# Optimization experiments

Measured on AMD Instinct MI355X. Metric: run time of the kernel, lower is better.

The kernel has to match this reference:

```python
import jax, jax.numpy as jnp
import numpy as np

B, S, D, H = 4, 2048, 1024, 16
Dh = D // H


def _layernorm(x, a, b):
    # torch.var default is unbiased (ddof=1)
    mu = jnp.mean(x, axis=-1, keepdims=True)
    sg = jnp.var(x, axis=-1, keepdims=True, ddof=1)
    return (x - mu) / jnp.sqrt(sg + 1e-08) * a + b


def setup_inputs() -> dict:
    key = jax.random.key(0)
    ks = jax.random.split(key, 16)
    s = 1.0 / np.sqrt(D)
    inp = {
        'q': jax.random.normal(ks[0], (B, S, D), jnp.float32),
        'k': jax.random.normal(ks[1], (B, S, D), jnp.float32),
        'v': jax.random.normal(ks[2], (B, S, D), jnp.float32),
        'g': jax.random.normal(ks[3], (B, S, D), jnp.float32),
        # causal mask: True = masked
        'm': jnp.triu(jnp.ones((S, S), jnp.bool_), k=1)[None, None],
        'Wq': jax.random.uniform(ks[4], (D, D), jnp.float32, -s, s),
        'bq': jnp.zeros((D,), jnp.float32),
        'Wk': jax.random.uniform(ks[5], (D, D), jnp.float32, -s, s),
        'bk': jnp.zeros((D,), jnp.float32),
        'Wv': jax.random.uniform(ks[6], (D, D), jnp.float32, -s, s),
        'bv': jnp.zeros((D,), jnp.float32),
        'Wg': jax.random.uniform(ks[7], (D, D), jnp.float32, -s, s),
        'bg': jnp.zeros((D,), jnp.float32),
        'ln_a': jnp.ones((D,), jnp.float32),
        'ln_b': jnp.zeros((D,), jnp.float32),
        'Wo': jax.random.uniform(ks[8], (D, D), jnp.float32, -s, s),
        'bo': jnp.zeros((D,), jnp.float32),
    }
    return inp


def reference(q, k, v, g, m, Wq, bq, Wk, bk, Wv, bv, Wg, bg, ln_a, ln_b, Wo, bo):
    qp = q @ Wq.T + bq
    kp = k @ Wk.T + bk
    vp = v @ Wv.T + bv
    gp = g @ Wg.T + bg
    # gating path: exact GELU (torch default), then custom LayerNorm (unbiased var)
    vp = jax.nn.gelu(vp, approximate=False)
    gp = jax.nn.gelu(gp, approximate=False)
    vp = _layernorm(vp, ln_a, ln_b)
    # [B,S,D] -> [B,H,S,Dh]
    qh = qp.reshape(B, S, H, Dh).transpose(0, 2, 1, 3)
    kh = kp.reshape(B, S, H, Dh).transpose(0, 2, 1, 3)
    vh = vp.reshape(B, S, H, Dh).transpose(0, 2, 1, 3)
    gh = gp.reshape(B, S, H, Dh).transpose(0, 2, 1, 3)
    a = jnp.einsum('bhqd,bhkd->bhqk', qh, kh) / jnp.sqrt(jnp.float32(Dh))
    a = jnp.where(m, -jnp.inf, a)
    a = jax.nn.softmax(a, axis=-1)
    # dropout = 0.0 (inference): no-op
    o = jnp.einsum('bhqk,bhkd->bhqd', a, vh)
    o = o * gh
    o = o.transpose(0, 2, 1, 3).reshape(B, S, D)
    o = o @ Wo.T + bo
    return (o, a)
```

## Files before the change

### kernel.cpp

```cpp
#include <hip/hip_runtime.h>
#include <hip/hip_bf16.h>
#include <cstdint>
#include <cstddef>

#define DEVINL static __device__ __forceinline__

typedef short bf16x8 __attribute__((ext_vector_type(8)));
typedef short s16x4  __attribute__((ext_vector_type(4)));
typedef float f32x4  __attribute__((ext_vector_type(4)));
typedef unsigned short u16;

static constexpr int Bb = 4, Ss = 2048, Dd = 1024, Hh = 16;
static constexpr int Mrows = Bb * Ss;
static constexpr int BHc = Bb * Hh;

DEVINL u16 f2bf(float f) {
    union { float f; uint32_t u; } v; v.f = f;
    uint32_t r = v.u + 0x7fffu + ((v.u >> 16) & 1u);
    return (u16)(r >> 16);
}
DEVINL float bf2f(u16 h) {
    union { uint32_t u; float f; } v; v.u = ((uint32_t)h) << 16;
    return v.f;
}
DEVINL float gelu_exact(float x) {
    return 0.5f * x * (1.0f + erff(x * 0.70710678118654752f));
}
DEVINL void gload16(const u16* gsrc, u16* ldsdst) {
    auto* g = reinterpret_cast<const __attribute__((address_space(1))) uint32_t*>(
        reinterpret_cast<uintptr_t>(gsrc));
    auto* l = reinterpret_cast<__attribute__((address_space(3))) uint32_t*>(
        reinterpret_cast<uintptr_t>(ldsdst));
    __builtin_amdgcn_global_load_lds(g, l, 16, 0, 0);
}

__global__ __launch_bounds__(256) void k_cvt_in(
    const float* __restrict__ s0, const float* __restrict__ s1,
    const float* __restrict__ s2, const float* __restrict__ s3,
    u16* __restrict__ d0, u16* __restrict__ d1,
    u16* __restrict__ d2, u16* __restrict__ d3, int n4) {
    int t = blockIdx.x * 256 + threadIdx.x;
    if (t >= n4) return;
    const float* s; u16* d;
    switch (blockIdx.y) {
        case 0: s = s0; d = d0; break;
        case 1: s = s1; d = d1; break;
        case 2: s = s2; d = d2; break;
        default: s = s3; d = d3; break;
    }
    float4 v = ((const float4*)s)[t];
    ushort4 o;
    o.x = f2bf(v.x); o.y = f2bf(v.y); o.z = f2bf(v.z); o.w = f2bf(v.w);
    ((ushort4*)d)[t] = o;
}

__global__ __launch_bounds__(256) void k_cvt_w(
    const float* __restrict__ s0, const float* __restrict__ s1,
    const float* __restrict__ s2, const float* __restrict__ s3,
    const float* __restrict__ s4,
    u16* __restrict__ d0, u16* __restrict__ d1, u16* __restrict__ d2,
    u16* __restrict__ d3, u16* __restrict__ d4, int n4) {
    int t = blockIdx.x * 256 + threadIdx.x;
    if (t >= n4) return;
    const float* s; u16* d;
    switch (blockIdx.y) {
        case 0: s = s0; d = d0; break;
        case 1: s = s1; d = d1; break;
        case 2: s = s2; d = d2; break;
        case 3: s = s3; d = d3; break;
        default: s = s4; d = d4; break;
    }
    float4 v = ((const float4*)s)[t];
    ushort4 o;
    o.x = f2bf(v.x); o.y = f2bf(v.y); o.z = f2bf(v.z); o.w = f2bf(v.w);
    ((ushort4*)d)[t] = o;
}

__global__ __launch_bounds__(256) void k_proj(
    const u16* __restrict__ qb, const u16* __restrict__ kb,
    const u16* __restrict__ vb, const u16* __restrict__ gb,
    const u16* __restrict__ Wqb, const u16* __restrict__ Wkb,
    const u16* __restrict__ Wvb, const u16* __restrict__ Wgb,
    const float* __restrict__ bqp, const float* __restrict__ bkp,
    const float* __restrict__ bvp, const float* __restrict__ bgp,
    u16* __restrict__ qp, u16* __restrict__ kpo,
    float* __restrict__ vp, u16* __restrict__ ghb)
{
    __shared__ u16 As[128 * 32];
    __shared__ u16 Bs[128 * 32];
    const int tid = threadIdx.x, lane = tid & 63, w = tid >> 6;
    const int wm = w >> 1, wn = w & 1;
    const int g = lane >> 4, li = lane & 15;
    const int orig = blockIdx.x;
    const int lid = (orig & 7) * 256 + (orig >> 3);
    const int z = lid >> 9, rem = lid & 511;
    const int m0 = (rem >> 3) * 128, n0 = (rem & 7) * 128;

    const u16 *Ap, *Wp; const float* bias;
    switch (z) {
        case 0: Ap = qb; Wp = Wqb; bias = bqp; break;
        case 1: Ap = kb; Wp = Wkb; bias = bkp; break;
        case 2: Ap = vb; Wp = Wvb; bias = bvp; break;
        default: Ap = gb; Wp = Wgb; bias = bgp; break;
    }

    const f32x4 zero4 = {0.f, 0.f, 0.f, 0.f};
    f32x4 acc[4][4];
#pragma unroll
    for (int m = 0; m < 4; m++)
#pragma unroll
        for (int n = 0; n < 4; n++) acc[m][n] = zero4;

    for (int k0 = 0; k0 < 1024; k0 += 32) {
        __syncthreads();
#pragma unroll
        for (int i = 0; i < 2; i++) {
            int chunk = (w * 2 + i) * 64 + lane;
            int row = chunk >> 2, cp = chunk & 3;
            gload16(Ap + (size_t)(m0 + row) * 1024 + k0 + ((cp ^ ((row >> 1) & 3)) << 3),
                    &As[(w * 2 + i) * 512]);
        }
#pragma unroll
        for (int i = 0; i < 2; i++) {
            int chunk = (w * 2 + i) * 64 + lane;
            int row = chunk >> 2, cp = chunk & 3;
            gload16(Wp + (size_t)(n0 + row) * 1024 + k0 + ((cp ^ ((row >> 1) & 3)) << 3),
                    &Bs[(w * 2 + i) * 512]);
        }
        __syncthreads();

        bf16x8 af[4], bfr[4];
#pragma unroll
        for (int m = 0; m < 4; m++) {
            int row = wm * 64 + m * 16 + li;
            af[m] = *(const bf16x8*)&As[row * 32 + ((g ^ ((row >> 1) & 3)) << 3)];
        }
#pragma unroll
        for (int n = 0; n < 4; n++) {
            int row = wn * 64 + n * 16 + li;
            bfr[n] = *(const bf16x8*)&Bs[row * 32 + ((g ^ ((row >> 1) & 3)) << 3)];
        }
#pragma unroll
        for (int m = 0; m < 4; m++)
#pragma unroll
            for (int n = 0; n < 4; n++)
                acc[m][n] = __builtin_amdgcn_mfma_f32_16x16x32_bf16(af[m], bfr[n], acc[m][n], 0, 0, 0);
    }

#pragma unroll
    for (int m = 0; m < 4; m++) {
#pragma unroll
        for (int n = 0; n < 4; n++) {
            int col = n0 + wn * 64 + n * 16 + li;
            float bv = bias[col];
#pragma unroll
            for (int r = 0; r < 4; r++) {
                int row = m0 + wm * 64 + m * 16 + g * 4 + r;
                float v = acc[m][n][r] + bv;
                size_t idx = (size_t)row * 1024 + col;
                if (z == 0)      qp[idx]  = f2bf(v);
                else if (z == 1) kpo[idx] = f2bf(v);
                else if (z == 2) vp[idx]  = gelu_exact(v);
                else             ghb[idx] = f2bf(gelu_exact(v));
            }
        }
    }
}

__global__ __launch_bounds__(256) void k_gemm_f(
    const u16* __restrict__ Ap, const u16* __restrict__ Wp,
    const float* __restrict__ bias, float* __restrict__ Cp)
{
    __shared__ u16 As[128 * 32];
    __shared__ u16 Bs[128 * 32];
    const int tid = threadIdx.x, lane = tid & 63, w = tid >> 6;
    const int wm = w >> 1, wn = w & 1;
    const int g = lane >> 4, li = lane & 15;
    const int orig = blockIdx.x;
    const int lid = (orig & 7) * 64 + (orig >> 3);
    const int m0 = (lid >> 3) * 128, n0 = (lid & 7) * 128;

    const f32x4 zero4 = {0.f, 0.f, 0.f, 0.f};
    f32x4 acc[4][4];
#pragma unroll
    for (int m = 0; m < 4; m++)
#pragma unroll
        for (int n = 0; n < 4; n++) acc[m][n] = zero4;

    for (int k0 = 0; k0 < 1024; k0 += 32) {
        __syncthreads();
#pragma unroll
        for (int i = 0; i < 2; i++) {
            int chunk = (w * 2 + i) * 64 + lane;
            int row = chunk >> 2, cp = chunk & 3;
            gload16(Ap + (size_t)(m0 + row) * 1024 + k0 + ((cp ^ ((row >> 1) & 3)) << 3),
                    &As[(w * 2 + i) * 512]);
        }
#pragma unroll
        for (int i = 0; i < 2; i++) {
            int chunk = (w * 2 + i) * 64 + lane;
            int row = chunk >> 2, cp = chunk & 3;
            gload16(Wp + (size_t)(n0 + row) * 1024 + k0 + ((cp ^ ((row >> 1) & 3)) << 3),
                    &Bs[(w * 2 + i) * 512]);
        }
        __syncthreads();

        bf16x8 af[4], bfr[4];
#pragma unroll
        for (int m = 0; m < 4; m++) {
            int row = wm * 64 + m * 16 + li;
            af[m] = *(const bf16x8*)&As[row * 32 + ((g ^ ((row >> 1) & 3)) << 3)];
        }
#pragma unroll
        for (int n = 0; n < 4; n++) {
            int row = wn * 64 + n * 16 + li;
            bfr[n] = *(const bf16x8*)&Bs[row * 32 + ((g ^ ((row >> 1) & 3)) << 3)];
        }
#pragma unroll
        for (int m = 0; m < 4; m++)
#pragma unroll
            for (int n = 0; n < 4; n++)
                acc[m][n] = __builtin_amdgcn_mfma_f32_16x16x32_bf16(af[m], bfr[n], acc[m][n], 0, 0, 0);
    }

#pragma unroll
    for (int m = 0; m < 4; m++) {
#pragma unroll
        for (int n = 0; n < 4; n++) {
            int col = n0 + wn * 64 + n * 16 + li;
            float bv = bias[col];
#pragma unroll
            for (int r = 0; r < 4; r++) {
                int row = m0 + wm * 64 + m * 16 + g * 4 + r;
                Cp[(size_t)row * 1024 + col] = acc[m][n][r] + bv;
            }
        }
    }
}

__global__ __launch_bounds__(256) void k_ln(const float* __restrict__ vp,
                                            const float* __restrict__ la,
                                            const float* __restrict__ lb,
                                            u16* __restrict__ vh) {
    int row = blockIdx.x;
    const float* x = vp + (size_t)row * 1024;
    int tid = threadIdx.x;
    float4 v = ((const float4*)x)[tid];
    float s = v.x + v.y + v.z + v.w;
    float s2 = v.x * v.x + v.y * v.y + v.z * v.z + v.w * v.w;
#pragma unroll
    for (int off = 1; off < 64; off <<= 1) {
        s  += __shfl_xor(s, off, 64);
        s2 += __shfl_xor(s2, off, 64);
    }
    __shared__ float red[8];
    int w = tid >> 6, lane = tid & 63;
    if (lane == 0) { red[w] = s; red[4 + w] = s2; }
    __syncthreads();
    s  = red[0] + red[1] + red[2] + red[3];
    s2 = red[4] + red[5] + red[6] + red[7];
    float mu = s * (1.0f / 1024.0f);
    float var = (s2 - 1024.0f * mu * mu) * (1.0f / 1023.0f);
    float rs = rsqrtf(var + 1e-8f);
    float4 a4 = ((const float4*)la)[tid];
    float4 b4 = ((const float4*)lb)[tid];
    ushort4 o;
    o.x = f2bf((v.x - mu) * rs * a4.x + b4.x);
    o.y = f2bf((v.y - mu) * rs * a4.y + b4.y);
    o.z = f2bf((v.z - mu) * rs * a4.z + b4.z);
    o.w = f2bf((v.w - mu) * rs * a4.w + b4.w);
    ((ushort4*)(vh + (size_t)row * 1024))[tid] = o;
}

__global__ __launch_bounds__(256) void k_transpose(const u16* __restrict__ vh,
                                                   u16* __restrict__ vhT) {
    int bh = blockIdx.y, b = bh >> 4, h = bh & 15, s0 = blockIdx.x * 64;
    __shared__ u16 t[64 * 96];
    int tid = threadIdx.x;
#pragma unroll
    for (int j = 0; j < 2; j++) {
        int u = j * 256 + tid;
        int r = u >> 3, c8 = u & 7;
        bf16x8 v = *(const bf16x8*)(vh + ((size_t)(b * 2048 + s0 + r) * 1024 + h * 64 + c8 * 8));
        *(bf16x8*)&t[r * 96 + c8 * 8] = v;
    }
    __syncthreads();
#pragma unroll
    for (int j = 0; j < 2; j++) {
        int u = j * 256 + tid;
        int d = u >> 3, s8 = u & 7;
        bf16x8 vv;
#pragma unroll
        for (int jj = 0; jj < 8; jj++) vv[jj] = (short)t[(s8 * 8 + jj) * 96 + d];
        *(bf16x8*)(vhT + ((size_t)(bh * 64 + d) * 2048 + s0 + s8 * 8)) = vv;
    }
}

__global__ __launch_bounds__(512) void k_attn(const u16* __restrict__ qp,
                                              const u16* __restrict__ kp,
                                              const u16* __restrict__ vhT,
                                              const u16* __restrict__ gh,
                                              float* __restrict__ aout,
                                              u16* __restrict__ gated) {
    __shared__ short Ps[8 * 16 * 128];
    const int tid = threadIdx.x, lane = tid & 63, w = tid >> 6;
    const int g = lane >> 4, li = lane & 15;
    const int orig = blockIdx.x;
    const int lid = (orig & 7) * 64 + (orig >> 3);
    const int bh = lid >> 3, i0 = lid & 7;
    const int b = bh >> 4, h = bh & 15;
    const u16* kbh = kp + ((size_t)(b * 2048) * 1024 + h * 64);
    const u16* vbh = vhT + (size_t)bh * 64 * 2048;
    const u16* ghb_base = gh + (size_t)(b * 2048) * 1024 + h * 64;
    float* arow = aout + (size_t)bh * 2048 * 2048;
    short* Pw = &Ps[w * 2048];
    const f32x4 zero4 = {0.f, 0.f, 0.f, 0.f};

    for (int half = 0; half < 2; ++half) {
        const int bx = half ? (15 - i0) : i0;
        const int q0 = bx * 128;
        const int qrow0 = q0 + w * 16;
        const int qrow = qrow0 + li;
        const u16* qbase = qp + ((size_t)(b * 2048 + qrow) * 1024 + h * 64 + g * 8);
        bf16x8 qa0 = *(const bf16x8*)qbase;
        bf16x8 qa1 = *(const bf16x8*)(qbase + 32);

        for (int kt = bx + 1; kt < 16; ++kt) {
            float* tbase = arow + (size_t)q0 * 2048 + kt * 128;
#pragma unroll
            for (int i = 0; i < 8; i++) {
                int u = i * 512 + tid;
                int row = u >> 5, cu = u & 31;
                __builtin_nontemporal_store(zero4, (f32x4*)(tbase + (size_t)row * 2048 + cu * 4));
            }
        }

        float l_run = 0.f;
        for (int kt = 0; kt <= bx; ++kt) {
            const int k0 = kt * 128;
#pragma unroll
            for (int n = 0; n < 8; n++) {
                int rb = k0 + n * 16 + li;
                const u16* krow = kbh + (size_t)rb * 1024 + g * 8;
                bf16x8 kb0 = *(const bf16x8*)krow;
                bf16x8 kb1 = *(const bf16x8*)(krow + 32);
                f32x4 c = zero4;
                c = __builtin_amdgcn_mfma_f32_16x16x32_bf16(kb0, qa0, c, 0, 0, 0);
                c = __builtin_amdgcn_mfma_f32_16x16x32_bf16(kb1, qa1, c, 0, 0, 0);
#pragma unroll
                for (int r = 0; r < 4; r++) {
                    int col = k0 + n * 16 + g * 4 + r;
                    l_run += (col <= qrow) ? __expf(c[r] * 0.125f) : 0.0f;
                }
            }
        }
        l_run += __shfl_xor(l_run, 16, 64);
        l_run += __shfl_xor(l_run, 32, 64);
        const float linv = 1.0f / l_run;

        f32x4 oacc[4];
#pragma unroll
        for (int n = 0; n < 4; n++) oacc[n] = zero4;
        for (int kt = 0; kt <= bx; ++kt) {
            const int k0 = kt * 128;
#pragma unroll
            for (int n = 0; n < 8; n++) {
                int rb = k0 + n * 16 + li;
                const u16* krow = kbh + (size_t)rb * 1024 + g * 8;
                bf16x8 kb0 = *(const bf16x8*)krow;
                bf16x8 kb1 = *(const bf16x8*)(krow + 32);
                f32x4 c = zero4;
                c = __builtin_amdgcn_mfma_f32_16x16x32_bf16(kb0, qa0, c, 0, 0, 0);
                c = __builtin_amdgcn_mfma_f32_16x16x32_bf16(kb1, qa1, c, 0, 0, 0);
#pragma unroll
                for (int r = 0; r < 4; r++) {
                    int col = k0 + n * 16 + g * 4 + r;
                    c[r] = (col <= qrow) ? __expf(c[r] * 0.125f) * linv : 0.0f;
                }
                __builtin_nontemporal_store(c,
                    (f32x4*)(arow + (size_t)qrow * 2048 + k0 + n * 16 + g * 4));
                s16x4 pk;
#pragma unroll
                for (int r = 0; r < 4; r++) pk[r] = (short)f2bf(c[r]);
                int chunk = n * 2 + (g >> 1);
                *(s16x4*)&Pw[li * 128 + ((chunk ^ (li & 7)) << 3) + (g & 1) * 4] = pk;
            }
#pragma unroll
            for (int ks = 0; ks < 4; ++ks) {
                int cl = ks * 4 + g;
                bf16x8 pa = *(const bf16x8*)&Pw[li * 128 + ((cl ^ (li & 7)) << 3)];
#pragma unroll
                for (int n = 0; n < 4; n++) {
                    int vr = n * 16 + li;
                    bf16x8 vb = *(const bf16x8*)(vbh + (size_t)vr * 2048 + k0 + cl * 8);
                    oacc[n] = __builtin_amdgcn_mfma_f32_16x16x32_bf16(pa, vb, oacc[n], 0, 0, 0);
                }
            }
        }

#pragma unroll
        for (int n = 0; n < 4; n++) {
            int d8 = n * 2 + (li >> 3), wi = li & 7;
#pragma unroll
            for (int r = 0; r < 4; r++) {
                int lr = g * 4 + r;
                Pw[lr * 64 + ((d8 ^ (lr & 7)) << 3) + wi] = (short)f2bf(oacc[n][r]);
            }
        }
#pragma unroll
        for (int it = 0; it < 2; ++it) {
            int lr = it * 8 + (lane >> 3);
            int c8 = lane & 7;
            int rowq = qrow0 + lr;
            bf16x8 ov = *(const bf16x8*)&Pw[lr * 64 + ((c8 ^ (lr & 7)) << 3)];
            bf16x8 gv = *(const bf16x8*)(ghb_base + (size_t)rowq * 1024 + c8 * 8);
            bf16x8 outv;
#pragma unroll
            for (int j = 0; j < 8; j++)
                outv[j] = (short)f2bf(bf2f((u16)ov[j]) * bf2f((u16)gv[j]));
            *(bf16x8*)(gated + ((size_t)(b * 2048 + rowq)) * 1024 + h * 64 + c8 * 8) = outv;
        }
    }
}

extern "C" void kernel_launch(void* const* d_in, const int* in_sizes, int n_in,
                              void* d_out, int out_size, void* d_ws, size_t ws_size,
                              hipStream_t stream) {
    const float* q  = (const float*)d_in[0];
    const float* k  = (const float*)d_in[1];
    const float* v  = (const float*)d_in[2];
    const float* g  = (const float*)d_in[3];
    const float* Wq = (const float*)d_in[5];
    const float* bq = (const float*)d_in[6];
    const float* Wk = (const float*)d_in[7];
    const float* bk = (const float*)d_in[8];
    const float* Wv = (const float*)d_in[9];
    const float* bv = (const float*)d_in[10];
    const float* Wg = (const float*)d_in[11];
    const float* bg = (const float*)d_in[12];
    const float* ln_a = (const float*)d_in[13];
    const float* ln_b = (const float*)d_in[14];
    const float* Wo = (const float*)d_in[15];
    const float* bo = (const float*)d_in[16];

    float* o_out = (float*)d_out;
    float* a_out = o_out + (size_t)Mrows * Dd;

    u16* qp    = (u16*)d_ws;
    u16* kpb   = qp    + (size_t)Mrows * Dd;
    u16* vhT   = kpb   + (size_t)Mrows * Dd;
    u16* ghb   = vhT   + (size_t)Mrows * Dd;
    u16* gated = ghb   + (size_t)Mrows * Dd;
    u16* Wo_bf = gated + (size_t)Mrows * Dd;

    u16* Wq_bf = (u16*)a_out;
    u16* Wk_bf = Wq_bf + (size_t)Dd * Dd;
    u16* Wv_bf = Wk_bf + (size_t)Dd * Dd;
    u16* Wg_bf = Wv_bf + (size_t)Dd * Dd;
    u16* qb    = Wg_bf + (size_t)Dd * Dd;
    u16* kb2   = qb    + (size_t)Mrows * Dd;
    u16* vb    = kb2   + (size_t)Mrows * Dd;
    u16* gb    = vb    + (size_t)Mrows * Dd;
    float* vp  = (float*)(gb + (size_t)Mrows * Dd);
    u16* vh    = (u16*)(vp + (size_t)Mrows * Dd);

    {
        int n4w = Dd * Dd / 4;
        dim3 gw((n4w + 255) / 256, 5);
        k_cvt_w<<<gw, 256, 0, stream>>>(Wq, Wk, Wv, Wg, Wo,
                                        Wq_bf, Wk_bf, Wv_bf, Wg_bf, Wo_bf, n4w);
        int n4i = Mrows * Dd / 4;
        dim3 gi((n4i + 255) / 256, 4);
        k_cvt_in<<<gi, 256, 0, stream>>>(q, k, v, g, qb, kb2, vb, gb, n4i);
    }

    k_proj<<<2048, 256, 0, stream>>>(qb, kb2, vb, gb,
                                     Wq_bf, Wk_bf, Wv_bf, Wg_bf,
                                     bq, bk, bv, bg,
                                     qp, kpb, vp, ghb);

    k_ln<<<Mrows, 256, 0, stream>>>(vp, ln_a, ln_b, vh);

    dim3 gt(Ss / 64, BHc);
    k_transpose<<<gt, 256, 0, stream>>>(vh, vhT);

    k_attn<<<512, 512, 0, stream>>>(qp, kpb, vhT, ghb, a_out, gated);

    k_gemm_f<<<512, 256, 0, stream>>>(gated, Wo_bf, bo, o_out);
}
```

Before: 672.6 us.

## Stage fp32 attention probs in LDS for coalesced row stores; skip mask on full tiles

The probability tile is now staged in padded fp32 shared memory, so the attention-matrix writes go out as full contiguous 512-byte row segments instead of scattered 16-byte pieces. Conversion to bf16 for the PV MFMA is moved to the read side. Tiles that lie fully below the diagonal skip the causal mask compare. The output accumulator is also kept in fp32 before gating, which drops one rounding step. The cost is a larger LDS footprint (about 70KB per block, which may limit occupancy) plus extra LDS traffic and conversions.

```diff
diff --git a/kernel.cpp b/kernel.cpp
--- a/kernel.cpp
+++ b/kernel.cpp
@@ -13,6 +13,7 @@
 static constexpr int Bb = 4, Ss = 2048, Dd = 1024, Hh = 16;
 static constexpr int Mrows = Bb * Ss;
 static constexpr int BHc = Bb * Hh;
+static constexpr int PSTR = 140;
 
 DEVINL u16 f2bf(float f) {
     union { float f; uint32_t u; } v; v.f = f;
@@ -302,7 +303,7 @@
                                               const u16* __restrict__ gh,
                                               float* __restrict__ aout,
                                               u16* __restrict__ gated) {
-    __shared__ short Ps[8 * 16 * 128];
+    extern __shared__ float PF[];
     const int tid = threadIdx.x, lane = tid & 63, w = tid >> 6;
     const int g = lane >> 4, li = lane & 15;
     const int orig = blockIdx.x;
@@ -313,7 +314,7 @@
     const u16* vbh = vhT + (size_t)bh * 64 * 2048;
     const u16* ghb_base = gh + (size_t)(b * 2048) * 1024 + h * 64;
     float* arow = aout + (size_t)bh * 2048 * 2048;
-    short* Pw = &Ps[w * 2048];
+    float* PW = PF + w * (16 * PSTR);
     const f32x4 zero4 = {0.f, 0.f, 0.f, 0.f};
 
     for (int half = 0; half < 2; ++half) {
@@ -338,6 +339,7 @@
         float l_run = 0.f;
         for (int kt = 0; kt <= bx; ++kt) {
             const int k0 = kt * 128;
+            const bool full = (kt < bx);
 #pragma unroll
             for (int n = 0; n < 8; n++) {
                 int rb = k0 + n * 16 + li;
@@ -347,10 +349,15 @@
                 f32x4 c = zero4;
                 c = __builtin_amdgcn_mfma_f32_16x16x32_bf16(kb0, qa0, c, 0, 0, 0);
                 c = __builtin_amdgcn_mfma_f32_16x16x32_bf16(kb1, qa1, c, 0, 0, 0);
-#pragma unroll
-                for (int r = 0; r < 4; r++) {
-                    int col = k0 + n * 16 + g * 4 + r;
-                    l_run += (col <= qrow) ? __expf(c[r] * 0.125f) : 0.0f;
+                if (full) {
+#pragma unroll
+                    for (int r = 0; r < 4; r++) l_run += __expf(c[r] * 0.125f);
+                } else {
+#pragma unroll
+                    for (int r = 0; r < 4; r++) {
+                        int col = k0 + n * 16 + g * 4 + r;
+                        l_run += (col <= qrow) ? __expf(c[r] * 0.125f) : 0.0f;
+                    }
                 }
             }
         }
@@ -363,6 +370,7 @@
         for (int n = 0; n < 4; n++) oacc[n] = zero4;
         for (int kt = 0; kt <= bx; ++kt) {
             const int k0 = kt * 128;
+            const bool full = (kt < bx);
 #pragma unroll
             for (int n = 0; n < 8; n++) {
                 int rb = k0 + n * 16 + li;
@@ -372,23 +380,37 @@
                 f32x4 c = zero4;
                 c = __builtin_amdgcn_mfma_f32_16x16x32_bf16(kb0, qa0, c, 0, 0, 0);
                 c = __builtin_amdgcn_mfma_f32_16x16x32_bf16(kb1, qa1, c, 0, 0, 0);
-#pragma unroll
-                for (int r = 0; r < 4; r++) {
-                    int col = k0 + n * 16 + g * 4 + r;
-                    c[r] = (col <= qrow) ? __expf(c[r] * 0.125f) * linv : 0.0f;
+                if (full) {
+#pragma unroll
+                    for (int r = 0; r < 4; r++) c[r] = __expf(c[r] * 0.125f) * linv;
+                } else {
+#pragma unroll
+                    for (int r = 0; r < 4; r++) {
+                        int col = k0 + n * 16 + g * 4 + r;
+                        c[r] = (col <= qrow) ? __expf(c[r] * 0.125f) * linv : 0.0f;
+                    }
                 }
-                __builtin_nontemporal_store(c,
-                    (f32x4*)(arow + (size_t)qrow * 2048 + k0 + n * 16 + g * 4));
-                s16x4 pk;
-#pragma unroll
-                for (int r = 0; r < 4; r++) pk[r] = (short)f2bf(c[r]);
-                int chunk = n * 2 + (g >> 1);
-                *(s16x4*)&Pw[li * 128 + ((chunk ^ (li & 7)) << 3) + (g & 1) * 4] = pk;
+                *(f32x4*)&PW[li * PSTR + n * 16 + g * 4] = c;
+            }
+#pragma unroll
+            for (int it = 0; it < 8; ++it) {
+                int row = it * 2 + (lane >> 5);
+                int c4 = lane & 31;
+                f32x4 val = *(const f32x4*)&PW[row * PSTR + c4 * 4];
+                __builtin_nontemporal_store(val,
+                    (f32x4*)(arow + (size_t)(qrow0 + row) * 2048 + k0 + c4 * 4));
             }
 #pragma unroll
             for (int ks = 0; ks < 4; ++ks) {
                 int cl = ks * 4 + g;
-                bf16x8 pa = *(const bf16x8*)&Pw[li * 128 + ((cl ^ (li & 7)) << 3)];
+                f32x4 lo = *(const f32x4*)&PW[li * PSTR + cl * 8];
+                f32x4 hi = *(const f32x4*)&PW[li * PSTR + cl * 8 + 4];
+                bf16x8 pa;
+#pragma unroll
+                for (int j = 0; j < 4; j++) {
+                    pa[j]     = (short)f2bf(lo[j]);
+                    pa[4 + j] = (short)f2bf(hi[j]);
+                }
 #pragma unroll
                 for (int n = 0; n < 4; n++) {
                     int vr = n * 16 + li;
@@ -400,11 +422,10 @@
 
 #pragma unroll
         for (int n = 0; n < 4; n++) {
-            int d8 = n * 2 + (li >> 3), wi = li & 7;
 #pragma unroll
             for (int r = 0; r < 4; r++) {
                 int lr = g * 4 + r;
-                Pw[lr * 64 + ((d8 ^ (lr & 7)) << 3) + wi] = (short)f2bf(oacc[n][r]);
+                PW[lr * PSTR + n * 16 + li] = oacc[n][r];
             }
         }
 #pragma unroll
@@ -412,12 +433,15 @@
             int lr = it * 8 + (lane >> 3);
             int c8 = lane & 7;
             int rowq = qrow0 + lr;
-            bf16x8 ov = *(const bf16x8*)&Pw[lr * 64 + ((c8 ^ (lr & 7)) << 3)];
+            f32x4 olo = *(const f32x4*)&PW[lr * PSTR + c8 * 8];
+            f32x4 ohi = *(const f32x4*)&PW[lr * PSTR + c8 * 8 + 4];
             bf16x8 gv = *(const bf16x8*)(ghb_base + (size_t)rowq * 1024 + c8 * 8);
             bf16x8 outv;
 #pragma unroll
-            for (int j = 0; j < 8; j++)
-                outv[j] = (short)f2bf(bf2f((u16)ov[j]) * bf2f((u16)gv[j]));
+            for (int j = 0; j < 4; j++) {
+                outv[j]     = (short)f2bf(olo[j] * bf2f((u16)gv[j]));
+                outv[4 + j] = (short)f2bf(ohi[j] * bf2f((u16)gv[4 + j]));
+            }
             *(bf16x8*)(gated + ((size_t)(b * 2048 + rowq)) * 1024 + h * 64 + c8 * 8) = outv;
         }
     }
@@ -484,7 +508,8 @@
     dim3 gt(Ss / 64, BHc);
     k_transpose<<<gt, 256, 0, stream>>>(vh, vhT);
 
-    k_attn<<<512, 512, 0, stream>>>(qp, kpb, vhT, ghb, a_out, gated);
+    size_t attn_lds = 8 * 16 * PSTR * sizeof(float);
+    k_attn<<<512, 512, attn_lds, stream>>>(qp, kpb, vhT, ghb, a_out, gated);
 
     k_gemm_f<<<512, 256, 0, stream>>>(gated, Wo_bf, bo, o_out);
 }
```

New measurement: 660.0 us. No clear change (-1.9%).
